# Performance work log

Hardware: AMD Instinct MI355X
Metric: run time of the kernel (lower is better)

## Reference

```python
import jax, jax.numpy as jnp
import numpy as np

S, B, C = 7, 2, 20
L_OBJ, L_NOBJ = 5.0, 0.5
EPS = 1e-06


def setup_inputs() -> dict:
    key = jax.random.key(0)
    k1, k2, k3 = jax.random.split(key, 3)
    N = 16384
    pred = jax.random.normal(k1, (N, S, S, B * 5 + C), dtype=jnp.float32)
    tgt = jax.random.uniform(k2, (N, S, S, 5 + C), dtype=jnp.float32)
    # objectness flag must be exactly 0.0 or 1.0 (loss tests true_box[0] == 1)
    obj = (jax.random.uniform(k3, (N, S, S)) < 0.3).astype(jnp.float32)
    target = tgt.at[..., 0].set(obj)
    return {"pred": pred, "target": target}


def _iou(cx1, cy1, w1, h1, cx2, cy2, w2, h2):
    # center-format boxes -> IoU (broadcasts over trailing B dim)
    b1x1, b1y1, b1x2, b1y2 = cx1 - w1 / 2, cy1 - h1 / 2, cx1 + w1 / 2, cy1 + h1 / 2
    b2x1, b2y1, b2x2, b2y2 = cx2 - w2 / 2, cy2 - h2 / 2, cx2 + w2 / 2, cy2 + h2 / 2
    iw = jnp.clip(jnp.minimum(b1x2, b2x2) - jnp.maximum(b1x1, b2x1), 0.0)
    ih = jnp.clip(jnp.minimum(b1y2, b2y2) - jnp.maximum(b1y1, b2y1), 0.0)
    inter = iw * ih
    a1 = (b1x2 - b1x1) * (b1y2 - b1y1)
    a2 = (b2x2 - b2x1) * (b2y2 - b2y1)
    return inter / (a1 + a2 - inter + EPS)


def _yolo_loss(pred, target):
    N = pred.shape[0]
    pb = pred[..., : B * 5].reshape(N, S, S, B, 5)          # [N,S,S,B,5]
    pcls = pred[..., B * 5:]                                 # [N,S,S,C]
    tconf = target[..., 0]                                   # [N,S,S]
    tx, ty, tw, th = target[..., 1], target[..., 2], target[..., 3], target[..., 4]
    tcls = target[..., 5:]                                   # [N,S,S,C]

    i_idx = jnp.arange(S, dtype=pred.dtype)[None, :, None]   # row index i
    j_idx = jnp.arange(S, dtype=pred.dtype)[None, None, :]   # col index j

    # absolute pred boxes [N,S,S,B]
    p_conf = pb[..., 0]
    p_x = (j_idx[..., None] + pb[..., 1]) / S
    p_y = (i_idx[..., None] + pb[..., 2]) / S
    p_w = jax.nn.relu(pb[..., 3])
    p_h = jax.nn.relu(pb[..., 4])

    # absolute true box [N,S,S,1] for broadcast vs B
    t_x = ((j_idx + tx) / S)[..., None]
    t_y = ((i_idx + ty) / S)[..., None]
    t_w_raw = tw[..., None]
    t_h_raw = th[..., None]

    # obj branch: true box with raw w/h ; noobj branch: relu'd (is_pred=True)
    iou_obj = _iou(p_x, p_y, p_w, p_h, t_x, t_y, t_w_raw, t_h_raw)            # [N,S,S,B]
    iou_no = _iou(p_x, p_y, p_w, p_h, t_x, t_y, jax.nn.relu(t_w_raw), jax.nn.relu(t_h_raw))

    def gather_best(arr, idx):
        return jnp.take_along_axis(arr, idx[..., None], axis=-1)[..., 0]

    # ---- object cells ----
    best_o = jnp.argmax(iou_obj, axis=-1)                    # [N,S,S]
    bx = gather_best(pb[..., 1], best_o)
    by = gather_best(pb[..., 2], best_o)
    bw = jax.nn.relu(gather_best(pb[..., 3], best_o))
    bh = jax.nn.relu(gather_best(pb[..., 4], best_o))
    bconf_o = gather_best(p_conf, best_o)
    biou = jax.lax.stop_gradient(gather_best(iou_obj, best_o))

    xy_loss = (bx - tx) ** 2 + (by - ty) ** 2
    wh_loss = (jnp.sqrt(jnp.abs(bw + EPS)) - jnp.sqrt(jnp.abs(tw + EPS))) ** 2 + \
              (jnp.sqrt(jnp.abs(bh + EPS)) - jnp.sqrt(jnp.abs(th + EPS))) ** 2
    conf_obj = (jax.nn.sigmoid(bconf_o) - biou) ** 2
    class_loss = jnp.sum((jax.nn.softmax(pcls, axis=-1) - tcls) ** 2, axis=-1)
    loss_obj = L_OBJ * (xy_loss + wh_loss) + conf_obj + class_loss

    # ---- no-object cells ----
    best_n = jnp.argmax(iou_no, axis=-1)
    bconf_n = gather_best(p_conf, best_n)
    loss_noobj = L_NOBJ * jax.nn.sigmoid(bconf_n) ** 2

    obj_mask = tconf == 1.0
    total = jnp.sum(jnp.where(obj_mask, loss_obj, loss_noobj))
    return total / N


def reference(pred, target):
    return _yolo_loss(pred, target)
```

## Files before the change

### kernel.cpp

```cpp
#include <hip/hip_runtime.h>

#define SS 7
#define NB 2
#define NC 20
#define PRED_W 30
#define TGT_W  25
#define BLOCK  256

constexpr float L_OBJ  = 5.0f;
constexpr float L_NOBJ = 0.5f;
constexpr float EPSV   = 1e-6f;

typedef float f4a8 __attribute__((ext_vector_type(4), aligned(8)));
typedef float f4a4 __attribute__((ext_vector_type(4), aligned(4)));
typedef float f2a8 __attribute__((ext_vector_type(2), aligned(8)));

__device__ __forceinline__ float sigmoidf_(float x) {
    return 1.0f / (1.0f + __expf(-x));
}

__device__ __forceinline__ float iou_(float cx1, float cy1, float w1, float h1,
                                      float cx2, float cy2, float w2, float h2) {
    float b1x1 = cx1 - w1 * 0.5f, b1y1 = cy1 - h1 * 0.5f;
    float b1x2 = cx1 + w1 * 0.5f, b1y2 = cy1 + h1 * 0.5f;
    float b2x1 = cx2 - w2 * 0.5f, b2y1 = cy2 - h2 * 0.5f;
    float b2x2 = cx2 + w2 * 0.5f, b2y2 = cy2 + h2 * 0.5f;
    float iw = fmaxf(fminf(b1x2, b2x2) - fmaxf(b1x1, b2x1), 0.0f);
    float ih = fmaxf(fminf(b1y2, b2y2) - fmaxf(b1y1, b2y1), 0.0f);
    float inter = iw * ih;
    float a1 = (b1x2 - b1x1) * (b1y2 - b1y1);
    float a2 = (b2x2 - b2x1) * (b2y2 - b2y1);
    return inter / (a1 + a2 - inter + EPSV);
}

__global__ __launch_bounds__(BLOCK) void yolo_loss_kernel(
        const float* __restrict__ pred,
        const float* __restrict__ target,
        float* __restrict__ partial,
        int ncells) {
    int cell = blockIdx.x * blockDim.x + threadIdx.x;
    float loss = 0.0f;

    if (cell < ncells) {
        int ij = cell % (SS * SS);
        int i  = ij / SS;
        int j  = ij % SS;

        float p[PRED_W];
        {
            const float* pb = pred + (size_t)cell * PRED_W;
            #pragma unroll
            for (int k = 0; k < 7; ++k) {
                f4a8 v = *reinterpret_cast<const f4a8*>(pb + 4 * k);
                p[4 * k]     = v.x;
                p[4 * k + 1] = v.y;
                p[4 * k + 2] = v.z;
                p[4 * k + 3] = v.w;
            }
            f2a8 v = *reinterpret_cast<const f2a8*>(pb + 28);
            p[28] = v.x;
            p[29] = v.y;
        }

        const float* tp = target + (size_t)cell * TGT_W;
        float tconf, tx, ty, tw, th;
        {
            f4a4 v = *reinterpret_cast<const f4a4*>(tp);
            tconf = v.x; tx = v.y; ty = v.z; tw = v.w;
            th = tp[4];
        }

        const bool is_obj = (tconf == 1.0f);

        float tcls[NC];
        if (is_obj) {
            #pragma unroll
            for (int k = 0; k < NC / 4; ++k) {
                f4a4 v = *reinterpret_cast<const f4a4*>(tp + 5 + 4 * k);
                tcls[4 * k]     = v.x;
                tcls[4 * k + 1] = v.y;
                tcls[4 * k + 2] = v.z;
                tcls[4 * k + 3] = v.w;
            }
        } else {
            #pragma unroll
            for (int k = 0; k < NC; ++k) tcls[k] = 0.0f;
        }

        float fi = (float)i, fj = (float)j;
        const float invS = 1.0f / (float)SS;

        float t_x = (fj + tx) * invS;
        float t_y = (fi + ty) * invS;

        float iou_b[NB];
        #pragma unroll
        for (int b = 0; b < NB; ++b) {
            float px = (fj + p[b * 5 + 1]) * invS;
            float py = (fi + p[b * 5 + 2]) * invS;
            float pw = fmaxf(p[b * 5 + 3], 0.0f);
            float ph = fmaxf(p[b * 5 + 4], 0.0f);
            iou_b[b] = iou_(px, py, pw, ph, t_x, t_y, tw, th);
        }

        int best = (iou_b[1] > iou_b[0]) ? 1 : 0;

        float bconf = p[best * 5 + 0];
        float bx    = p[best * 5 + 1];
        float by    = p[best * 5 + 2];
        float bw    = fmaxf(p[best * 5 + 3], 0.0f);
        float bh    = fmaxf(p[best * 5 + 4], 0.0f);
        float biou  = iou_b[best];

        float dx = bx - tx, dy = by - ty;
        float xy_loss = dx * dx + dy * dy;

        float sw = sqrtf(fabsf(bw + EPSV)) - sqrtf(fabsf(tw + EPSV));
        float sh = sqrtf(fabsf(bh + EPSV)) - sqrtf(fabsf(th + EPSV));
        float wh_loss = sw * sw + sh * sh;

        float dc = sigmoidf_(bconf) - biou;
        float conf_obj = dc * dc;

        float m = p[NB * 5];
        #pragma unroll
        for (int k = 1; k < NC; ++k) m = fmaxf(m, p[NB * 5 + k]);
        float esum = 0.0f;
        float e[NC];
        #pragma unroll
        for (int k = 0; k < NC; ++k) {
            e[k] = __expf(p[NB * 5 + k] - m);
            esum += e[k];
        }
        float inv_esum = 1.0f / esum;
        float class_loss = 0.0f;
        #pragma unroll
        for (int k = 0; k < NC; ++k) {
            float d = e[k] * inv_esum - tcls[k];
            class_loss += d * d;
        }

        float loss_obj = L_OBJ * (xy_loss + wh_loss) + conf_obj + class_loss;

        float sn = sigmoidf_(bconf);
        float loss_noobj = L_NOBJ * sn * sn;

        loss = is_obj ? loss_obj : loss_noobj;
    }

    #pragma unroll
    for (int off = 32; off > 0; off >>= 1)
        loss += __shfl_down(loss, off, 64);

    __shared__ float wsum[BLOCK / 64];
    int lane = threadIdx.x & 63;
    int wid  = threadIdx.x >> 6;
    if (lane == 0) wsum[wid] = loss;
    __syncthreads();
    if (threadIdx.x == 0) {
        partial[blockIdx.x] = wsum[0] + wsum[1] + wsum[2] + wsum[3];
    }
}

__global__ __launch_bounds__(BLOCK) void reduce_kernel(
        const float* __restrict__ partial, float* __restrict__ out,
        int nblocks, float inv_n) {
    float s = 0.0f;
    for (int idx = threadIdx.x; idx < nblocks; idx += BLOCK)
        s += partial[idx];

    #pragma unroll
    for (int off = 32; off > 0; off >>= 1)
        s += __shfl_down(s, off, 64);

    __shared__ float wsum[BLOCK / 64];
    int lane = threadIdx.x & 63;
    int wid  = threadIdx.x >> 6;
    if (lane == 0) wsum[wid] = s;
    __syncthreads();
    if (threadIdx.x == 0)
        out[0] = (wsum[0] + wsum[1] + wsum[2] + wsum[3]) * inv_n;
}

extern "C" void kernel_launch(void* const* d_in, const int* in_sizes, int n_in,
                              void* d_out, int out_size, void* d_ws, size_t ws_size,
                              hipStream_t stream) {
    const float* pred   = (const float*)d_in[0];
    const float* target = (const float*)d_in[1];
    float* out = (float*)d_out;
    float* partial = (float*)d_ws;

    int n = in_sizes[0] / (SS * SS * PRED_W);
    int ncells = n * SS * SS;
    float inv_n = 1.0f / (float)n;

    int grid = ncells / BLOCK;
    yolo_loss_kernel<<<grid, BLOCK, 0, stream>>>(pred, target, partial, ncells);
    reduce_kernel<<<1, BLOCK, 0, stream>>>(partial, out, grid, inv_n);
}
```

Baseline: 195.3 us.

## Stage pred and target rows through padded LDS with coalesced float4 loads

Each block now loads its contiguous slab of target and then pred with coalesced 16-byte loads into a shared buffer padded to odd strides, and each thread reads its own row from LDS. This replaces strided per-thread row loads, which touch many cache lines per wavefront. Target class values are now always read, even for no-object cells, and the softmax exponentials are recomputed rather than kept in registers. The cost is about 31 KB of LDS per block, extra barriers, and a launch-bounds occupancy hint.

```diff
diff --git a/kernel.cpp b/kernel.cpp
--- a/kernel.cpp
+++ b/kernel.cpp
@@ -6,14 +6,12 @@
 #define PRED_W 30
 #define TGT_W  25
 #define BLOCK  256
+#define PSTR   31
+#define TSTR   27
 
 constexpr float L_OBJ  = 5.0f;
 constexpr float L_NOBJ = 0.5f;
 constexpr float EPSV   = 1e-6f;
-
-typedef float f4a8 __attribute__((ext_vector_type(4), aligned(8)));
-typedef float f4a4 __attribute__((ext_vector_type(4), aligned(4)));
-typedef float f2a8 __attribute__((ext_vector_type(2), aligned(8)));
 
 __device__ __forceinline__ float sigmoidf_(float x) {
     return 1.0f / (1.0f + __expf(-x));
@@ -33,59 +31,80 @@
     return inter / (a1 + a2 - inter + EPSV);
 }
 
-__global__ __launch_bounds__(BLOCK) void yolo_loss_kernel(
+__global__ __launch_bounds__(BLOCK, 4) void yolo_loss_kernel(
         const float* __restrict__ pred,
         const float* __restrict__ target,
         float* __restrict__ partial,
         int ncells) {
-    int cell = blockIdx.x * blockDim.x + threadIdx.x;
+    __shared__ float sbuf[BLOCK * PSTR];
+    __shared__ float wsum[BLOCK / 64];
+
+    const int tid   = threadIdx.x;
+    const int cell0 = blockIdx.x * BLOCK;
+
+    {
+        const float4* g4 = reinterpret_cast<const float4*>(target + (size_t)cell0 * TGT_W);
+        #pragma unroll
+        for (int k = 0; k < 7; ++k) {
+            int idx = k * BLOCK + tid;
+            if (idx < (BLOCK * TGT_W) / 4) {
+                float4 v = g4[idx];
+                int f = idx * 4;
+                int r = f / TGT_W;
+                int c = f - r * TGT_W;
+                float vals[4] = {v.x, v.y, v.z, v.w};
+                #pragma unroll
+                for (int q = 0; q < 4; ++q) {
+                    int cc = c + q, rr = r;
+                    if (cc >= TGT_W) { cc -= TGT_W; rr += 1; }
+                    sbuf[rr * TSTR + cc] = vals[q];
+                }
+            }
+        }
+    }
+    __syncthreads();
+
+    float tconf, tx, ty, tw, th;
+    float tcls[NC];
+    {
+        const float* trow = sbuf + tid * TSTR;
+        tconf = trow[0]; tx = trow[1]; ty = trow[2]; tw = trow[3]; th = trow[4];
+        #pragma unroll
+        for (int k = 0; k < NC; ++k) tcls[k] = trow[5 + k];
+    }
+    __syncthreads();
+
+    {
+        const float4* g4 = reinterpret_cast<const float4*>(pred + (size_t)cell0 * PRED_W);
+        #pragma unroll
+        for (int k = 0; k < 8; ++k) {
+            int idx = k * BLOCK + tid;
+            if (idx < (BLOCK * PRED_W) / 4) {
+                float4 v = g4[idx];
+                int f = idx * 4;
+                int r = f / PRED_W;
+                int c = f - r * PRED_W;
+                float vals[4] = {v.x, v.y, v.z, v.w};
+                #pragma unroll
+                for (int q = 0; q < 4; ++q) {
+                    int cc = c + q, rr = r;
+                    if (cc >= PRED_W) { cc -= PRED_W; rr += 1; }
+                    sbuf[rr * PSTR + cc] = vals[q];
+                }
+            }
+        }
+    }
+    __syncthreads();
+
     float loss = 0.0f;
-
-    if (cell < ncells) {
+    {
+        const float* prow = sbuf + tid * PSTR;
+        int cell = cell0 + tid;
         int ij = cell % (SS * SS);
         int i  = ij / SS;
         int j  = ij % SS;
 
-        float p[PRED_W];
-        {
-            const float* pb = pred + (size_t)cell * PRED_W;
-            #pragma unroll
-            for (int k = 0; k < 7; ++k) {
-                f4a8 v = *reinterpret_cast<const f4a8*>(pb + 4 * k);
-                p[4 * k]     = v.x;
-                p[4 * k + 1] = v.y;
-                p[4 * k + 2] = v.z;
-                p[4 * k + 3] = v.w;
-            }
-            f2a8 v = *reinterpret_cast<const f2a8*>(pb + 28);
-            p[28] = v.x;
-            p[29] = v.y;
-        }
-
-        const float* tp = target + (size_t)cell * TGT_W;
-        float tconf, tx, ty, tw, th;
-        {
-            f4a4 v = *reinterpret_cast<const f4a4*>(tp);
-            tconf = v.x; tx = v.y; ty = v.z; tw = v.w;
-            th = tp[4];
-        }
-
         const bool is_obj = (tconf == 1.0f);
-
-        float tcls[NC];
-        if (is_obj) {
-            #pragma unroll
-            for (int k = 0; k < NC / 4; ++k) {
-                f4a4 v = *reinterpret_cast<const f4a4*>(tp + 5 + 4 * k);
-                tcls[4 * k]     = v.x;
-                tcls[4 * k + 1] = v.y;
-                tcls[4 * k + 2] = v.z;
-                tcls[4 * k + 3] = v.w;
-            }
-        } else {
-            #pragma unroll
-            for (int k = 0; k < NC; ++k) tcls[k] = 0.0f;
-        }
 
         float fi = (float)i, fj = (float)j;
         const float invS = 1.0f / (float)SS;
@@ -96,20 +115,20 @@
         float iou_b[NB];
         #pragma unroll
         for (int b = 0; b < NB; ++b) {
-            float px = (fj + p[b * 5 + 1]) * invS;
-            float py = (fi + p[b * 5 + 2]) * invS;
-            float pw = fmaxf(p[b * 5 + 3], 0.0f);
-            float ph = fmaxf(p[b * 5 + 4], 0.0f);
+            float px = (fj + prow[b * 5 + 1]) * invS;
+            float py = (fi + prow[b * 5 + 2]) * invS;
+            float pw = fmaxf(prow[b * 5 + 3], 0.0f);
+            float ph = fmaxf(prow[b * 5 + 4], 0.0f);
             iou_b[b] = iou_(px, py, pw, ph, t_x, t_y, tw, th);
         }
 
         int best = (iou_b[1] > iou_b[0]) ? 1 : 0;
 
-        float bconf = p[best * 5 + 0];
-        float bx    = p[best * 5 + 1];
-        float by    = p[best * 5 + 2];
-        float bw    = fmaxf(p[best * 5 + 3], 0.0f);
-        float bh    = fmaxf(p[best * 5 + 4], 0.0f);
+        float bconf = prow[best * 5 + 0];
+        float bx    = prow[best * 5 + 1];
+        float by    = prow[best * 5 + 2];
+        float bw    = fmaxf(prow[best * 5 + 3], 0.0f);
+        float bh    = fmaxf(prow[best * 5 + 4], 0.0f);
         float biou  = iou_b[best];
 
         float dx = bx - tx, dy = by - ty;
@@ -122,21 +141,17 @@
         float dc = sigmoidf_(bconf) - biou;
         float conf_obj = dc * dc;
 
-        float m = p[NB * 5];
-        #pragma unroll
-        for (int k = 1; k < NC; ++k) m = fmaxf(m, p[NB * 5 + k]);
+        float m = prow[NB * 5];
+        #pragma unroll
+        for (int k = 1; k < NC; ++k) m = fmaxf(m, prow[NB * 5 + k]);
         float esum = 0.0f;
-        float e[NC];
-        #pragma unroll
-        for (int k = 0; k < NC; ++k) {
-            e[k] = __expf(p[NB * 5 + k] - m);
-            esum += e[k];
-        }
+        #pragma unroll
+        for (int k = 0; k < NC; ++k) esum += __expf(prow[NB * 5 + k] - m);
         float inv_esum = 1.0f / esum;
         float class_loss = 0.0f;
         #pragma unroll
         for (int k = 0; k < NC; ++k) {
-            float d = e[k] * inv_esum - tcls[k];
+            float d = __expf(prow[NB * 5 + k] - m) * inv_esum - tcls[k];
             class_loss += d * d;
         }
 
@@ -146,13 +161,13 @@
         float loss_noobj = L_NOBJ * sn * sn;
 
         loss = is_obj ? loss_obj : loss_noobj;
+        if (cell >= ncells) loss = 0.0f;
     }
 
     #pragma unroll
     for (int off = 32; off > 0; off >>= 1)
         loss += __shfl_down(loss, off, 64);
 
-    __shared__ float wsum[BLOCK / 64];
     int lane = threadIdx.x & 63;
     int wid  = threadIdx.x >> 6;
     if (lane == 0) wsum[wid] = loss;
```

Result: no change. 199.0 us (+1.9%).

## Process four cells per thread with register prefetch of next cell

Applied to the files above, without the earlier changes.

Each thread now handles four cells strided by the block size and loads the next cell's prediction and target header into registers while computing the current one. The grid shrinks fourfold, and the softmax recomputes the exponentials instead of keeping a 20-element array. The aim is to hide memory latency in this bandwidth-bound loss and cut block count and partial sums. The cost is more registers, which may lower occupancy, and the kernel drops the bounds check, so it assumes the cell count divides evenly by 1024.

```diff
diff --git a/kernel.cpp b/kernel.cpp
--- a/kernel.cpp
+++ b/kernel.cpp
@@ -6,6 +6,7 @@
 #define PRED_W 30
 #define TGT_W  25
 #define BLOCK  256
+#define CELLS  4
 
 constexpr float L_OBJ  = 5.0f;
 constexpr float L_NOBJ = 0.5f;
@@ -33,84 +34,108 @@
     return inter / (a1 + a2 - inter + EPSV);
 }
 
-__global__ __launch_bounds__(BLOCK) void yolo_loss_kernel(
+#define LOAD_PRED(dst, cellidx)                                           \
+    {                                                                     \
+        const float* pb_ = pred + (size_t)(cellidx) * PRED_W;             \
+        _Pragma("unroll")                                                 \
+        for (int m_ = 0; m_ < 7; ++m_) {                                  \
+            f4a8 v_ = *reinterpret_cast<const f4a8*>(pb_ + 4 * m_);       \
+            dst[4 * m_]     = v_.x;                                       \
+            dst[4 * m_ + 1] = v_.y;                                       \
+            dst[4 * m_ + 2] = v_.z;                                       \
+            dst[4 * m_ + 3] = v_.w;                                       \
+        }                                                                 \
+        f2a8 w_ = *reinterpret_cast<const f2a8*>(pb_ + 28);               \
+        dst[28] = w_.x;                                                   \
+        dst[29] = w_.y;                                                   \
+    }
+
+#define LOAD_THEAD(c_, x_, y_, w_, h_, cellidx)                           \
+    {                                                                     \
+        const float* tp_ = target + (size_t)(cellidx) * TGT_W;            \
+        f4a4 v_ = *reinterpret_cast<const f4a4*>(tp_);                    \
+        c_ = v_.x; x_ = v_.y; y_ = v_.z; w_ = v_.w;                       \
+        h_ = tp_[4];                                                      \
+    }
+
+__global__ __launch_bounds__(BLOCK, 4) void yolo_loss_kernel(
         const float* __restrict__ pred,
         const float* __restrict__ target,
         float* __restrict__ partial,
         int ncells) {
-    int cell = blockIdx.x * blockDim.x + threadIdx.x;
+    const int tid  = threadIdx.x;
+    const int base = blockIdx.x * (BLOCK * CELLS);
+
     float loss = 0.0f;
 
-    if (cell < ncells) {
-        int ij = cell % (SS * SS);
-        int i  = ij / SS;
-        int j  = ij % SS;
-
-        float p[PRED_W];
+    float p[PRED_W];
+    float tconf, tx, ty, tw, th;
+    LOAD_PRED(p, base + tid);
+    LOAD_THEAD(tconf, tx, ty, tw, th, base + tid);
+
+    const float invS = 1.0f / (float)SS;
+
+    #pragma unroll
+    for (int k = 0; k < CELLS; ++k) {
+        const int cell = base + k * BLOCK + tid;
+
+        float pn[PRED_W];
+        float tcn, txn, tyn, twn, thn;
+        if (k < CELLS - 1) {
+            LOAD_PRED(pn, cell + BLOCK);
+            LOAD_THEAD(tcn, txn, tyn, twn, thn, cell + BLOCK);
+        }
+
+        const int ij = cell % (SS * SS);
+        const int i  = ij / SS;
+        const int j  = ij % SS;
+        const bool is_obj = (tconf == 1.0f);
+
+        float tcls[NC];
         {
-            const float* pb = pred + (size_t)cell * PRED_W;
-            #pragma unroll
-            for (int k = 0; k < 7; ++k) {
-                f4a8 v = *reinterpret_cast<const f4a8*>(pb + 4 * k);
-                p[4 * k]     = v.x;
-                p[4 * k + 1] = v.y;
-                p[4 * k + 2] = v.z;
-                p[4 * k + 3] = v.w;
+            const float* tp = target + (size_t)cell * TGT_W;
+            if (is_obj) {
+                #pragma unroll
+                for (int m = 0; m < NC / 4; ++m) {
+                    f4a4 v = *reinterpret_cast<const f4a4*>(tp + 5 + 4 * m);
+                    tcls[4 * m]     = v.x;
+                    tcls[4 * m + 1] = v.y;
+                    tcls[4 * m + 2] = v.z;
+                    tcls[4 * m + 3] = v.w;
+                }
+            } else {
+                #pragma unroll
+                for (int m = 0; m < NC; ++m) tcls[m] = 0.0f;
             }
-            f2a8 v = *reinterpret_cast<const f2a8*>(pb + 28);
-            p[28] = v.x;
-            p[29] = v.y;
-        }
-
-        const float* tp = target + (size_t)cell * TGT_W;
-        float tconf, tx, ty, tw, th;
-        {
-            f4a4 v = *reinterpret_cast<const f4a4*>(tp);
-            tconf = v.x; tx = v.y; ty = v.z; tw = v.w;
-            th = tp[4];
-        }
-
-        const bool is_obj = (tconf == 1.0f);
-
-        float tcls[NC];
-        if (is_obj) {
-            #pragma unroll
-            for (int k = 0; k < NC / 4; ++k) {
-                f4a4 v = *reinterpret_cast<const f4a4*>(tp + 5 + 4 * k);
-                tcls[4 * k]     = v.x;
-                tcls[4 * k + 1] = v.y;
-                tcls[4 * k + 2] = v.z;
-                tcls[4 * k + 3] = v.w;
-            }
-        } else {
-            #pragma unroll
-            for (int k = 0; k < NC; ++k) tcls[k] = 0.0f;
         }
 
         float fi = (float)i, fj = (float)j;
-        const float invS = 1.0f / (float)SS;
-
         float t_x = (fj + tx) * invS;
         float t_y = (fi + ty) * invS;
 
-        float iou_b[NB];
-        #pragma unroll
-        for (int b = 0; b < NB; ++b) {
-            float px = (fj + p[b * 5 + 1]) * invS;
-            float py = (fi + p[b * 5 + 2]) * invS;
-            float pw = fmaxf(p[b * 5 + 3], 0.0f);
-            float ph = fmaxf(p[b * 5 + 4], 0.0f);
-            iou_b[b] = iou_(px, py, pw, ph, t_x, t_y, tw, th);
-        }
-
-        int best = (iou_b[1] > iou_b[0]) ? 1 : 0;
-
-        float bconf = p[best * 5 + 0];
-        float bx    = p[best * 5 + 1];
-        float by    = p[best * 5 + 2];
-        float bw    = fmaxf(p[best * 5 + 3], 0.0f);
-        float bh    = fmaxf(p[best * 5 + 4], 0.0f);
-        float biou  = iou_b[best];
+        float iou0, iou1;
+        {
+            float px = (fj + p[1]) * invS;
+            float py = (fi + p[2]) * invS;
+            float pw = fmaxf(p[3], 0.0f);
+            float ph = fmaxf(p[4], 0.0f);
+            iou0 = iou_(px, py, pw, ph, t_x, t_y, tw, th);
+        }
+        {
+            float px = (fj + p[6]) * invS;
+            float py = (fi + p[7]) * invS;
+            float pw = fmaxf(p[8], 0.0f);
+            float ph = fmaxf(p[9], 0.0f);
+            iou1 = iou_(px, py, pw, ph, t_x, t_y, tw, th);
+        }
+
+        const bool b1 = (iou1 > iou0);
+        float bconf = b1 ? p[5] : p[0];
+        float bx    = b1 ? p[6] : p[1];
+        float by    = b1 ? p[7] : p[2];
+        float bw    = fmaxf(b1 ? p[8] : p[3], 0.0f);
+        float bh    = fmaxf(b1 ? p[9] : p[4], 0.0f);
+        float biou  = b1 ? iou1 : iou0;
 
         float dx = bx - tx, dy = by - ty;
         float xy_loss = dx * dx + dy * dy;
@@ -124,19 +149,15 @@
 
         float m = p[NB * 5];
         #pragma unroll
-        for (int k = 1; k < NC; ++k) m = fmaxf(m, p[NB * 5 + k]);
+        for (int q = 1; q < NC; ++q) m = fmaxf(m, p[NB * 5 + q]);
         float esum = 0.0f;
-        float e[NC];
         #pragma unroll
-        for (int k = 0; k < NC; ++k) {
-            e[k] = __expf(p[NB * 5 + k] - m);
-            esum += e[k];
-        }
+        for (int q = 0; q < NC; ++q) esum += __expf(p[NB * 5 + q] - m);
         float inv_esum = 1.0f / esum;
         float class_loss = 0.0f;
         #pragma unroll
-        for (int k = 0; k < NC; ++k) {
-            float d = e[k] * inv_esum - tcls[k];
+        for (int q = 0; q < NC; ++q) {
+            float d = __expf(p[NB * 5 + q] - m) * inv_esum - tcls[q];
             class_loss += d * d;
         }
 
@@ -145,7 +166,13 @@
         float sn = sigmoidf_(bconf);
         float loss_noobj = L_NOBJ * sn * sn;
 
-        loss = is_obj ? loss_obj : loss_noobj;
+        loss += is_obj ? loss_obj : loss_noobj;
+
+        if (k < CELLS - 1) {
+            #pragma unroll
+            for (int q = 0; q < PRED_W; ++q) p[q] = pn[q];
+            tconf = tcn; tx = txn; ty = tyn; tw = twn; th = thn;
+        }
     }
 
     #pragma unroll
@@ -194,7 +221,7 @@
     int ncells = n * SS * SS;
     float inv_n = 1.0f / (float)n;
 
-    int grid = ncells / BLOCK;
+    int grid = ncells / (BLOCK * CELLS);
     yolo_loss_kernel<<<grid, BLOCK, 0, stream>>>(pred, target, partial, ncells);
     reduce_kernel<<<1, BLOCK, 0, stream>>>(partial, out, grid, inv_n);
 }
```

Result: slower. 265.0 us (+35.7%).
